# Performance work log

Hardware: AMD Instinct MI355X
Metric: run time of the kernel (lower is better)

The kernel has to match this reference:

```python
import jax, jax.numpy as jnp
import numpy as np

VAR_NUM, IN_DIM, OUT_DIM = 3, 8, 32
N_PTS, M_PTS, K_LAST = 8192, 2048, 10
RADIUS = 0.0342
PROJ_HIDDEN = 64
N_DIM = 2
MLP_DIMS = [2 * N_DIM + OUT_DIM, 80, 80, OUT_DIM]  # [36, 80, 80, 32]


def _gelu(x):
    # torch F.gelu default = exact erf form
    return jax.nn.gelu(x, approximate=False)


def _radius_neighbors(data, queries, r):
    # CSR-style neighbor lists (indices grouped per query), chunked for memory
    idx_chunks = []
    counts = np.zeros(queries.shape[0], np.int64)
    r2 = r * r
    for s in range(0, queries.shape[0], 1024):
        q = queries[s:s + 1024]
        d2 = ((q[:, None, :] - data[None, :, :]) ** 2).sum(-1)
        mask = d2 <= r2
        _, cols = np.nonzero(mask)  # row-major -> grouped by query
        idx_chunks.append(cols.astype(np.int32))
        counts[s:s + q.shape[0]] = mask.sum(1)
    return np.concatenate(idx_chunks), counts.astype(np.int32)


def _knn(data, queries, k):
    out = np.zeros((queries.shape[0], k), np.int32)
    for s in range(0, queries.shape[0], 1024):
        q = queries[s:s + 1024]
        d2 = ((q[:, None, :] - data[None, :, :]) ** 2).sum(-1)
        out[s:s + q.shape[0]] = np.argpartition(d2, k, axis=1)[:, :k]
    return out.reshape(-1)


def _mlp_params(key, dims):
    Ws, bs = [], []
    for i in range(len(dims) - 1):
        key, k1 = jax.random.split(key)
        Ws.append(jax.random.normal(k1, (dims[i], dims[i + 1]), jnp.float32) / np.sqrt(dims[i]).astype(np.float32))
        bs.append(jnp.zeros((dims[i + 1],), jnp.float32))
    return Ws, bs


def setup_inputs():
    rng = np.random.default_rng(0)
    input_grid = rng.uniform(size=(N_PTS, N_DIM)).astype(np.float32)
    output_grid = rng.uniform(size=(M_PTS, N_DIM)).astype(np.float32)
    nbr_index, nbr_counts = _radius_neighbors(input_grid, input_grid, RADIUS)
    nbr_seg = np.repeat(np.arange(N_PTS, dtype=np.int32), nbr_counts)
    nbr_last_index = _knn(input_grid, output_grid, K_LAST)

    key = jax.random.key(0)
    ks = jax.random.split(key, 4)
    inp = jax.random.normal(ks[0], (1, N_PTS, VAR_NUM * IN_DIM), jnp.float32)
    pW, pb = _mlp_params(ks[1], [IN_DIM, PROJ_HIDDEN, OUT_DIM])
    it0_W, it0_b = _mlp_params(ks[2], MLP_DIMS)
    it1_W, it1_b = _mlp_params(ks[3], MLP_DIMS)
    return dict(
        inp=inp,
        input_grid=jnp.asarray(input_grid), output_grid=jnp.asarray(output_grid),
        proj_W0=pW[0], proj_b0=pb[0], proj_W1=pW[1], proj_b1=pb[1],
        it0_W0=it0_W[0], it0_b0=it0_b[0], it0_W1=it0_W[1], it0_b1=it0_b[1], it0_W2=it0_W[2], it0_b2=it0_b[2],
        it1_W0=it1_W[0], it1_b0=it1_b[0], it1_W1=it1_W[1], it1_b1=it1_b[1], it1_W2=it1_W[2], it1_b2=it1_b[2],
        nbr_index=jnp.asarray(nbr_index), nbr_seg=jnp.asarray(nbr_seg),
        nbr_counts=jnp.asarray(nbr_counts), nbr_last_index=jnp.asarray(nbr_last_index),
    )


def _mlp3(x, W0, b0, W1, b1, W2, b2):
    x = _gelu(x @ W0 + b0)
    x = _gelu(x @ W1 + b1)
    return x @ W2 + b2


def reference(inp, input_grid, output_grid, proj_W0, proj_b0, proj_W1, proj_b1,
              it0_W0, it0_b0, it0_W1, it0_b1, it0_W2, it0_b2,
              it1_W0, it1_b0, it1_W1, it1_b1, it1_W2, it1_b2,
              nbr_index, nbr_seg, nbr_counts, nbr_last_index):
    B, N, _ = inp.shape  # B must be 1 (module's IT indexing assumes it)
    x = inp.reshape(B * N, VAR_NUM, IN_DIM)
    # pointwise projection MLP (gelu between layers)
    x = _gelu(x @ proj_W0 + proj_b0) @ proj_W1 + proj_b1  # (N, V, OUT_DIM)

    inv_counts = (1.0 / jnp.maximum(nbr_counts, 1).astype(x.dtype))[:, None]
    y_pos = input_grid[nbr_index]        # (E, 2) neighbor positions
    self_pos = input_grid[nbr_seg]       # (E, 2) query positions
    last_y = input_grid[nbr_last_index]                    # (M*K, 2)
    last_self = jnp.repeat(output_grid, K_LAST, axis=0)    # (M*K, 2)

    outs = []
    for v in range(VAR_NUM):
        f = x[:, v, :]
        # IT layer 0: radius neighborhoods on input grid, residual add
        agg = jnp.concatenate([y_pos, self_pos, f[nbr_index]], axis=-1)  # (E, 36)
        h = _mlp3(agg, it0_W0, it0_b0, it0_W1, it0_b1, it0_W2, it0_b2)
        f = jax.ops.segment_sum(h, nbr_seg, num_segments=N) * inv_counts + f
        # IT layer 1 (last): fixed-K neighbors from input grid to output grid, mean
        agg = jnp.concatenate([last_y, last_self, f[nbr_last_index]], axis=-1)
        h = _mlp3(agg, it1_W0, it1_b0, it1_W1, it1_b1, it1_W2, it1_b2)
        outs.append(h.reshape(M_PTS, K_LAST, OUT_DIM).mean(axis=1))
    # original concatenates temp[None] along dim=2 -> (1, M, V*OUT_DIM)
    return jnp.concatenate(outs, axis=-1)[None]
```

## Files before the change

kernel.cpp:

```cpp
#include <hip/hip_runtime.h>
#include <hip/hip_bf16.h>
#include <math.h>

#define N_PTS 8192
#define M_PTS 2048
#define KLAST 10
#define VARS 3
#define OUTD 32
#define D1 80
#define D2 80
#define PB 16
#define LPTS 4
#define NT 768
#define NWAVES 12
#define TPCH 104
#define W0P 72
#define W1P 104
#define RP 40

typedef float f4 __attribute__((ext_vector_type(4)));
typedef short bf16x8 __attribute__((ext_vector_type(8)));

__device__ __forceinline__ float gelu_f(float x) {
    float x2 = x * x;
    float t = x * (0.7978845608028654f + 0.0356774081f * x2);
    float u = __expf(2.0f * t);
    float th = 1.0f - 2.0f * __builtin_amdgcn_rcpf(u + 1.0f);
    return 0.5f * x * (1.0f + th);
}
__device__ __forceinline__ unsigned short f2bf(float x) {
    unsigned int u = __float_as_uint(x);
    u += 0x7FFF + ((u >> 16) & 1);
    return (unsigned short)(u >> 16);
}
__device__ __forceinline__ float bf2f(unsigned short h) {
    return __uint_as_float(((unsigned int)h) << 16);
}
__device__ __forceinline__ int pk2(float a, float b) {
    __hip_bfloat162 h = __float22bfloat162_rn(float2{a, b});
    int r; __builtin_memcpy(&r, &h, 4); return r;
}

__device__ __forceinline__ void stage_weights(
    unsigned short* W0h, unsigned short* W1h, unsigned short* W2h, float* bs,
    const float* __restrict__ W0g, const float* __restrict__ b0g,
    const float* __restrict__ W1g, const float* __restrict__ b1g,
    const float* __restrict__ W2g, const float* __restrict__ b2g, int t)
{
    for (int idx = t; idx < D1 * W0P; idx += NT) {
        int col = idx / W0P, k = idx - col * W0P;
        float w = (k < 32) ? W0g[(k + 4) * D1 + col]
                           : ((k < 36) ? W0g[(k - 32) * D1 + col] : 0.0f);
        W0h[idx] = f2bf(w);
    }
    for (int idx = t; idx < D1 * W1P; idx += NT) {
        int col = idx / W1P, k = idx - col * W1P;
        W1h[idx] = f2bf((k < D2) ? W1g[k * D1 + col] : 0.0f);
    }
    for (int idx = t; idx < OUTD * W1P; idx += NT) {
        int col = idx / W1P, k = idx - col * W1P;
        W2h[idx] = f2bf((k < D2) ? W2g[k * OUTD + col] : 0.0f);
    }
    for (int idx = t; idx < 192; idx += NT)
        bs[idx] = (idx < 80) ? b0g[idx] : (idx < 160 ? b1g[idx - 80] : b2g[idx - 160]);
}

__device__ __forceinline__ void mlp_chunk(
    int4 featsi, int4 posfi, unsigned short* Trow,
    const unsigned short* W0h, const unsigned short* W1h,
    const unsigned short* W2h, const float* bs, int lm, int quad)
{
    bf16x8 b1f0 = *(bf16x8*)&featsi;
    bf16x8 b1f1 = *(bf16x8*)&posfi;
#pragma unroll 1
    for (int cb = 0; cb < 5; ++cb) {
        f4 acc = *(const f4*)&bs[cb * 16 + quad * 4];
        bf16x8 a0 = *(const bf16x8*)&W0h[(cb * 16 + lm) * W0P + quad * 8];
        bf16x8 a1 = *(const bf16x8*)&W0h[(cb * 16 + lm) * W0P + 32 + quad * 8];
        acc = __builtin_amdgcn_mfma_f32_16x16x32_bf16(a0, b1f0, acc, 0, 0, 0);
        acc = __builtin_amdgcn_mfma_f32_16x16x32_bf16(a1, b1f1, acc, 0, 0, 0);
        *(int2*)&Trow[cb * 16 + quad * 4] =
            make_int2(pk2(gelu_f(acc.x), gelu_f(acc.y)),
                      pk2(gelu_f(acc.z), gelu_f(acc.w)));
    }
    bf16x8 b2f[3];
    b2f[0] = *(const bf16x8*)&Trow[quad * 8];
    b2f[1] = *(const bf16x8*)&Trow[32 + quad * 8];
    b2f[2] = *(const bf16x8*)&Trow[64 + quad * 8];
#pragma unroll 1
    for (int cb = 0; cb < 5; ++cb) {
        f4 acc = *(const f4*)&bs[80 + cb * 16 + quad * 4];
        const unsigned short* wh = &W1h[(cb * 16 + lm) * W1P + quad * 8];
        bf16x8 h0 = *(const bf16x8*)&wh[0];
        bf16x8 h1 = *(const bf16x8*)&wh[32];
        bf16x8 h2 = *(const bf16x8*)&wh[64];
        acc = __builtin_amdgcn_mfma_f32_16x16x32_bf16(h0, b2f[0], acc, 0, 0, 0);
        acc = __builtin_amdgcn_mfma_f32_16x16x32_bf16(h1, b2f[1], acc, 0, 0, 0);
        acc = __builtin_amdgcn_mfma_f32_16x16x32_bf16(h2, b2f[2], acc, 0, 0, 0);
        *(int2*)&Trow[cb * 16 + quad * 4] =
            make_int2(pk2(gelu_f(acc.x), gelu_f(acc.y)),
                      pk2(gelu_f(acc.z), gelu_f(acc.w)));
    }
    bf16x8 b3f[3];
    b3f[0] = *(const bf16x8*)&Trow[quad * 8];
    b3f[1] = *(const bf16x8*)&Trow[32 + quad * 8];
    b3f[2] = *(const bf16x8*)&Trow[64 + quad * 8];
    float* po = (float*)Trow;
#pragma unroll 1
    for (int cb = 0; cb < 2; ++cb) {
        f4 acc = *(const f4*)&bs[160 + cb * 16 + quad * 4];
        const unsigned short* wh = &W2h[(cb * 16 + lm) * W1P + quad * 8];
        bf16x8 h0 = *(const bf16x8*)&wh[0];
        bf16x8 h1 = *(const bf16x8*)&wh[32];
        bf16x8 h2 = *(const bf16x8*)&wh[64];
        acc = __builtin_amdgcn_mfma_f32_16x16x32_bf16(h0, b3f[0], acc, 0, 0, 0);
        acc = __builtin_amdgcn_mfma_f32_16x16x32_bf16(h1, b3f[1], acc, 0, 0, 0);
        acc = __builtin_amdgcn_mfma_f32_16x16x32_bf16(h2, b3f[2], acc, 0, 0, 0);
        *(f4*)&po[cb * 16 + quad * 4] = acc;
    }
}

__global__ __launch_bounds__(1024) void scan_kernel(
    const int* __restrict__ counts, int* __restrict__ offsets)
{
    __shared__ int wtot[16], wexc[16];
    const int t = threadIdx.x, lane = t & 63, wave = t >> 6;
    int4 a = ((const int4*)counts)[2 * t];
    int4 b = ((const int4*)counts)[2 * t + 1];
    int e1 = a.x, e2 = e1 + a.y, e3 = e2 + a.z, e4 = e3 + a.w;
    int e5 = e4 + b.x, e6 = e5 + b.y, e7 = e6 + b.z;
    int s = e7 + b.w;
    int x = s;
#pragma unroll
    for (int d = 1; d < 64; d <<= 1) {
        int y = __shfl_up(x, d);
        if (lane >= d) x += y;
    }
    if (lane == 63) wtot[wave] = x;
    int lane_base = x - s;
    __syncthreads();
    if (wave == 0 && lane < 16) {
        int v = wtot[lane];
        int xx = v;
#pragma unroll
        for (int d = 1; d < 16; d <<= 1) {
            int y = __shfl_up(xx, d);
            if (lane >= d) xx += y;
        }
        wexc[lane] = xx - v;
    }
    __syncthreads();
    int base = wexc[wave] + lane_base;
    ((int4*)offsets)[2 * t]     = make_int4(base, base + e1, base + e2, base + e3);
    ((int4*)offsets)[2 * t + 1] = make_int4(base + e4, base + e5, base + e6, base + e7);
}

__global__ __launch_bounds__(256) void proj_kernel(
    const float* __restrict__ inp, const float* __restrict__ grid_in,
    const float* __restrict__ W0, const float* __restrict__ b0,
    const float* __restrict__ W1, const float* __restrict__ b1,
    unsigned short* __restrict__ f0b)
{
    __shared__ float W0s[8 * 64];
    __shared__ float W1s[64 * OUTD];
    __shared__ float xs[32 * 8];
    __shared__ float H[32 * 64];
    const int t = threadIdx.x;
    const int r0 = blockIdx.x * 32;
    for (int idx = t; idx < 512; idx += 256) W0s[idx] = W0[idx];
    for (int idx = t; idx < 64 * OUTD; idx += 256) W1s[idx] = W1[idx];
    xs[t] = inp[r0 * 8 + t];
    if (t < 32) {
        int row = r0 + t, n = row / 3, v = row - n * 3;
        *(int*)(f0b + ((size_t)(v << 13) + n) * RP + 32) =
            pk2(grid_in[2 * n], grid_in[2 * n + 1]);
    }
    __syncthreads();
#pragma unroll 1
    for (int p = 0; p < 8; ++p) {
        int o = t + 256 * p, r = o >> 6, col = o & 63;
        float s = b0[col];
#pragma unroll
        for (int k = 0; k < 8; ++k) s += xs[r * 8 + k] * W0s[k * 64 + col];
        H[o] = gelu_f(s);
    }
    __syncthreads();
#pragma unroll 1
    for (int p = 0; p < 4; ++p) {
        int o = t + 256 * p, r = o >> 5, c = o & 31;
        float s = b1[c];
#pragma unroll 8
        for (int k = 0; k < 64; ++k) s += H[r * 64 + k] * W1s[k * OUTD + c];
        int row = r0 + r;
        int n = row / 3, v = row - n * 3;
        f0b[((size_t)(v << 13) + n) * RP + c] = f2bf(s);
    }
}

__global__ __launch_bounds__(768, 6) void agg_kernel(
    const float* __restrict__ grid_in, const unsigned short* __restrict__ f0b,
    const int* __restrict__ nbr_index, const int* __restrict__ offsets,
    const int* __restrict__ counts,
    const float* __restrict__ W0g, const float* __restrict__ b0g,
    const float* __restrict__ W1g, const float* __restrict__ b1g,
    const float* __restrict__ W2g, const float* __restrict__ b2g,
    unsigned short* __restrict__ f1b)
{
    __shared__ __attribute__((aligned(16))) unsigned short Tb[NWAVES * 16 * TPCH];
    __shared__ __attribute__((aligned(16))) unsigned short W0h[D1 * W0P];
    __shared__ __attribute__((aligned(16))) unsigned short W1h[D1 * W1P];
    __shared__ __attribute__((aligned(16))) unsigned short W2h[OUTD * W1P];
    __shared__ __attribute__((aligned(16))) float bs[192];
    __shared__ __attribute__((aligned(16))) float accH[VARS * PB * 32];
    __shared__ int offs[PB + 1];
    __shared__ int px2b[PB];
    __shared__ float invb[PB];

    const int t = threadIdx.x;
    const int lane = t & 63, wave = t >> 6;
    const int lm = lane & 15, quad = lane >> 4;
    const int p0 = blockIdx.x * PB;

    stage_weights(W0h, W1h, W2h, bs, W0g, b0g, W1g, b1g, W2g, b2g, t);
    if (t < PB) {
        offs[t] = offsets[p0 + t];
        int c = counts[p0 + t];
        invb[t] = 1.0f / (float)(c > 1 ? c : 1);
        px2b[t] = pk2(grid_in[2 * (p0 + t)], grid_in[2 * (p0 + t) + 1]);
    }
    if (t == PB) offs[PB] = offsets[p0 + PB - 1] + counts[p0 + PB - 1];
    for (int idx = t; idx < VARS * PB * 32; idx += NT) accH[idx] = 0.0f;
    __syncthreads();

    unsigned short* TbW = Tb + (wave * 16) * TPCH;
    if (lane < 32)
        *(int4*)(TbW + (lane >> 1) * TPCH + 80 + (lane & 1) * 8) = make_int4(0, 0, 0, 0);

    const int e0 = offs[0];
    const int cntT = offs[PB] - e0;
    const int Rb = VARS * cntT;
    const int nch = (Rb + 15) >> 4;

    unsigned short* Trow = TbW + lm * TPCH;

    int pkey; int4 pfeats, pposf;
    {
        int myrow = (wave << 4) + lm;
        pkey = -1; pfeats = make_int4(0,0,0,0); pposf = make_int4(0,0,0,0);
        if (myrow < Rb) {
            int myv = (myrow >= 2 * cntT) ? 2 : ((myrow >= cntT) ? 1 : 0);
            int e = e0 + myrow - myv * cntT;
            int myj = nbr_index[e];
            int lp = 0;
#pragma unroll
            for (int l = 1; l < PB; ++l) lp += (e >= offs[l]);
            pkey = myv * PB + lp;
            const unsigned short* rec = f0b + ((size_t)(myv << 13) + myj) * RP;
            pfeats = ((const int4*)rec)[quad];
            if (quad == 0) pposf = make_int4(*(const int*)(rec + 32), px2b[lp], 0, 0);
        }
    }

    for (int ch = wave; ch < nch; ch += NWAVES) {
        int ckey = pkey; int4 cfeats = pfeats, cposf = pposf;
        int nc = ch + NWAVES;
        pkey = -1; pfeats = make_int4(0,0,0,0); pposf = make_int4(0,0,0,0);
        if (nc < nch) {
            int myrow = (nc << 4) + lm;
            if (myrow < Rb) {
                int myv = (myrow >= 2 * cntT) ? 2 : ((myrow >= cntT) ? 1 : 0);
                int e = e0 + myrow - myv * cntT;
                int myj = nbr_index[e];
                int lp = 0;
#pragma unroll
                for (int l = 1; l < PB; ++l) lp += (e >= offs[l]);
                pkey = myv * PB + lp;
                const unsigned short* rec = f0b + ((size_t)(myv << 13) + myj) * RP;
                pfeats = ((const int4*)rec)[quad];
                if (quad == 0) pposf = make_int4(*(const int*)(rec + 32), px2b[lp], 0, 0);
            }
        }
        if (ckey < 0) { cfeats = make_int4(0,0,0,0); cposf = make_int4(0,0,0,0); }
        mlp_chunk(cfeats, cposf, Trow, W0h, W1h, W2h, bs, lm, quad);
        int col = lane & 31, eo = lane >> 5;
#pragma unroll 1
        for (int e2 = eo; e2 < 16; e2 += 2) {
            int k = __shfl(ckey, e2);
            if (k >= 0)
                atomicAdd(&accH[k * 32 + col], ((const float*)(TbW + e2 * TPCH))[col]);
        }
    }
    __syncthreads();
    for (int idx = t; idx < VARS * PB * OUTD; idx += NT) {
        int key = idx >> 5, c = idx & 31;
        int v = key >> 4, lp = key & 15;
        size_t rec = ((size_t)(v << 13) + p0 + lp) * RP;
        float val = accH[key * 32 + c] * invb[lp] + bf2f(f0b[rec + c]);
        f1b[rec + c] = f2bf(val);
    }
    if (t < VARS * PB) {
        int v = t >> 4, lp = t & 15;
        *(int*)(f1b + ((size_t)(v << 13) + p0 + lp) * RP + 32) = px2b[lp];
    }
}

__global__ __launch_bounds__(768, 6) void last_kernel(
    const unsigned short* __restrict__ f1b, const float* __restrict__ grid_out,
    const int* __restrict__ nbr_last,
    const float* __restrict__ W0g, const float* __restrict__ b0g,
    const float* __restrict__ W1g, const float* __restrict__ b1g,
    const float* __restrict__ W2g, const float* __restrict__ b2g,
    float* __restrict__ out)
{
    __shared__ __attribute__((aligned(16))) unsigned short Tb[NWAVES * 16 * TPCH];
    __shared__ __attribute__((aligned(16))) unsigned short W0h[D1 * W0P];
    __shared__ __attribute__((aligned(16))) unsigned short W1h[D1 * W1P];
    __shared__ __attribute__((aligned(16))) unsigned short W2h[OUTD * W1P];
    __shared__ __attribute__((aligned(16))) float bs[192];
    __shared__ __attribute__((aligned(16))) float accH[LPTS * VARS * 32];
    __shared__ int pxo2b[LPTS];

    const int t = threadIdx.x;
    const int lane = t & 63, wave = t >> 6;
    const int lm = lane & 15, quad = lane >> 4;
    const int m0 = blockIdx.x * LPTS;

    stage_weights(W0h, W1h, W2h, bs, W0g, b0g, W1g, b1g, W2g, b2g, t);
    if (t < LPTS)
        pxo2b[t] = pk2(grid_out[2 * (m0 + t)], grid_out[2 * (m0 + t) + 1]);
    for (int idx = t; idx < LPTS * VARS * 32; idx += NT) accH[idx] = 0.0f;
    __syncthreads();
    unsigned short* TbW = Tb + (wave * 16) * TPCH;
    if (lane < 32)
        *(int4*)(TbW + (lane >> 1) * TPCH + 80 + (lane & 1) * 8) = make_int4(0, 0, 0, 0);

    const int Rb = LPTS * VARS * KLAST;
    const int nch = (Rb + 15) >> 4;
    unsigned short* Trow = TbW + lm * TPCH;

    for (int ch = wave; ch < nch; ch += NWAVES) {
        int myrow = (ch << 4) + lm;
        int ckey = -1; int4 cfeats = make_int4(0,0,0,0), cposf = make_int4(0,0,0,0);
        if (myrow < Rb) {
            int lp = myrow / 30, rr = myrow - lp * 30;
            int v = rr / KLAST, kk = rr - v * KLAST;
            int myj = nbr_last[(m0 + lp) * KLAST + kk];
            ckey = lp * VARS + v;
            const unsigned short* rec = f1b + ((size_t)(v << 13) + myj) * RP;
            cfeats = ((const int4*)rec)[quad];
            if (quad == 0) cposf = make_int4(*(const int*)(rec + 32), pxo2b[lp], 0, 0);
        }
        mlp_chunk(cfeats, cposf, Trow, W0h, W1h, W2h, bs, lm, quad);
        int col = lane & 31, eo = lane >> 5;
#pragma unroll 1
        for (int e2 = eo; e2 < 16; e2 += 2) {
            int k = __shfl(ckey, e2);
            if (k >= 0)
                atomicAdd(&accH[k * 32 + col], ((const float*)(TbW + e2 * TPCH))[col]);
        }
    }
    __syncthreads();
    if (t < LPTS * VARS * OUTD) {
        int key = t >> 5, c = t & 31;
        int lp = key / VARS, v = key - lp * VARS;
        out[((size_t)(m0 + lp) * VARS + v) * OUTD + c] = accH[key * 32 + c] * (1.0f / KLAST);
    }
}

extern "C" void kernel_launch(void* const* d_in, const int* in_sizes, int n_in,
                              void* d_out, int out_size, void* d_ws, size_t ws_size,
                              hipStream_t stream) {
    const float* inp      = (const float*)d_in[0];
    const float* grid_in  = (const float*)d_in[1];
    const float* grid_out = (const float*)d_in[2];
    const float* pW0 = (const float*)d_in[3];
    const float* pb0 = (const float*)d_in[4];
    const float* pW1 = (const float*)d_in[5];
    const float* pb1 = (const float*)d_in[6];
    const float* i0W0 = (const float*)d_in[7];
    const float* i0b0 = (const float*)d_in[8];
    const float* i0W1 = (const float*)d_in[9];
    const float* i0b1 = (const float*)d_in[10];
    const float* i0W2 = (const float*)d_in[11];
    const float* i0b2 = (const float*)d_in[12];
    const float* i1W0 = (const float*)d_in[13];
    const float* i1b0 = (const float*)d_in[14];
    const float* i1W1 = (const float*)d_in[15];
    const float* i1b1 = (const float*)d_in[16];
    const float* i1W2 = (const float*)d_in[17];
    const float* i1b2 = (const float*)d_in[18];
    const int* nbr_index  = (const int*)d_in[19];
    const int* nbr_counts = (const int*)d_in[21];
    const int* nbr_last   = (const int*)d_in[22];

    unsigned short* f0b = (unsigned short*)d_ws;
    unsigned short* f1b = f0b + (size_t)VARS * N_PTS * RP;
    int* offsets = (int*)(f1b + (size_t)VARS * N_PTS * RP);

    proj_kernel<<<(N_PTS * VARS) / 32, 256, 0, stream>>>(inp, grid_in, pW0, pb0, pW1, pb1, f0b);
    scan_kernel<<<1, 1024, 0, stream>>>(nbr_counts, offsets);
    agg_kernel<<<N_PTS / PB, NT, 0, stream>>>(grid_in, f0b, nbr_index, offsets, nbr_counts,
                                              i0W0, i0b0, i0W1, i0b1, i0W2, i0b2, f1b);
    last_kernel<<<M_PTS / LPTS, NT, 0, stream>>>(f1b, grid_out, nbr_last,
                                                 i1W0, i1b0, i1W1, i1b1, i1W2, i1b2,
                                                 (float*)d_out);
}
```

Before: 338.1 us.

## Fuse scan into projection kernel, simplify GELU, double points per last block

Folds the prefix-scan of neighbor counts into an extra block of the projection kernel, removing one kernel launch. Rewrites the tanh-GELU approximation with exp2 and fewer operations. Increases LPTS from 4 to 8 so each last-layer block handles more output points, halving its grid. Risks: the last_kernel's indexing must still be valid for LPTS=8, and the scan block serializes 32 counts per thread.

```diff
diff --git a/kernel.cpp b/kernel.cpp
--- a/kernel.cpp
+++ b/kernel.cpp
@@ -10,7 +10,7 @@
 #define D1 80
 #define D2 80
 #define PB 16
-#define LPTS 4
+#define LPTS 8
 #define NT 768
 #define NWAVES 12
 #define TPCH 104
@@ -23,10 +23,10 @@
 
 __device__ __forceinline__ float gelu_f(float x) {
     float x2 = x * x;
-    float t = x * (0.7978845608028654f + 0.0356774081f * x2);
-    float u = __expf(2.0f * t);
-    float th = 1.0f - 2.0f * __builtin_amdgcn_rcpf(u + 1.0f);
-    return 0.5f * x * (1.0f + th);
+    float s = x * __builtin_fmaf(0.1029418f, x2, 2.3022083f);
+    float u = __builtin_amdgcn_exp2f(s);
+    float r = __builtin_amdgcn_rcpf(u + 1.0f);
+    return __builtin_fmaf(-x, r, x);
 }
 __device__ __forceinline__ unsigned short f2bf(float x) {
     unsigned int u = __float_as_uint(x);
@@ -120,52 +120,55 @@
     }
 }
 
-__global__ __launch_bounds__(1024) void scan_kernel(
-    const int* __restrict__ counts, int* __restrict__ offsets)
-{
-    __shared__ int wtot[16], wexc[16];
-    const int t = threadIdx.x, lane = t & 63, wave = t >> 6;
-    int4 a = ((const int4*)counts)[2 * t];
-    int4 b = ((const int4*)counts)[2 * t + 1];
-    int e1 = a.x, e2 = e1 + a.y, e3 = e2 + a.z, e4 = e3 + a.w;
-    int e5 = e4 + b.x, e6 = e5 + b.y, e7 = e6 + b.z;
-    int s = e7 + b.w;
-    int x = s;
-#pragma unroll
-    for (int d = 1; d < 64; d <<= 1) {
-        int y = __shfl_up(x, d);
-        if (lane >= d) x += y;
-    }
-    if (lane == 63) wtot[wave] = x;
-    int lane_base = x - s;
-    __syncthreads();
-    if (wave == 0 && lane < 16) {
-        int v = wtot[lane];
-        int xx = v;
-#pragma unroll
-        for (int d = 1; d < 16; d <<= 1) {
-            int y = __shfl_up(xx, d);
-            if (lane >= d) xx += y;
-        }
-        wexc[lane] = xx - v;
-    }
-    __syncthreads();
-    int base = wexc[wave] + lane_base;
-    ((int4*)offsets)[2 * t]     = make_int4(base, base + e1, base + e2, base + e3);
-    ((int4*)offsets)[2 * t + 1] = make_int4(base + e4, base + e5, base + e6, base + e7);
-}
-
-__global__ __launch_bounds__(256) void proj_kernel(
+__global__ __launch_bounds__(256) void proj_scan_kernel(
     const float* __restrict__ inp, const float* __restrict__ grid_in,
     const float* __restrict__ W0, const float* __restrict__ b0,
     const float* __restrict__ W1, const float* __restrict__ b1,
-    unsigned short* __restrict__ f0b)
+    unsigned short* __restrict__ f0b,
+    const int* __restrict__ counts, int* __restrict__ offsets)
 {
+    const int t = threadIdx.x;
+    if (blockIdx.x == 768) {
+        __shared__ int ws2[4], wx2[4];
+        const int lane = t & 63, wave = t >> 6;
+        int4 a[8];
+#pragma unroll
+        for (int i = 0; i < 8; ++i) a[i] = ((const int4*)counts)[t * 8 + i];
+        int s = 0;
+#pragma unroll
+        for (int i = 0; i < 8; ++i) s += a[i].x + a[i].y + a[i].z + a[i].w;
+        int x = s;
+#pragma unroll
+        for (int d = 1; d < 64; d <<= 1) {
+            int y = __shfl_up(x, d);
+            if (lane >= d) x += y;
+        }
+        if (lane == 63) ws2[wave] = x;
+        __syncthreads();
+        if (t == 0) {
+            wx2[0] = 0;
+            wx2[1] = ws2[0];
+            wx2[2] = ws2[0] + ws2[1];
+            wx2[3] = ws2[0] + ws2[1] + ws2[2];
+        }
+        __syncthreads();
+        int base = wx2[wave] + (x - s);
+#pragma unroll
+        for (int i = 0; i < 8; ++i) {
+            int4 c = a[i];
+            int4 o;
+            o.x = base; base += c.x;
+            o.y = base; base += c.y;
+            o.z = base; base += c.z;
+            o.w = base; base += c.w;
+            ((int4*)offsets)[t * 8 + i] = o;
+        }
+        return;
+    }
     __shared__ float W0s[8 * 64];
     __shared__ float W1s[64 * OUTD];
     __shared__ float xs[32 * 8];
     __shared__ float H[32 * 64];
-    const int t = threadIdx.x;
     const int r0 = blockIdx.x * 32;
     for (int idx = t; idx < 512; idx += 256) W0s[idx] = W0[idx];
     for (int idx = t; idx < 64 * OUTD; idx += 256) W1s[idx] = W1[idx];
@@ -397,9 +400,10 @@
     unsigned short* f1b = f0b + (size_t)VARS * N_PTS * RP;
     int* offsets = (int*)(f1b + (size_t)VARS * N_PTS * RP);
 
-    proj_kernel<<<(N_PTS * VARS) / 32, 256, 0, stream>>>(inp, grid_in, pW0, pb0, pW1, pb1, f0b);
-    scan_kernel<<<1, 1024, 0, stream>>>(nbr_counts, offsets);
-    agg_kernel<<<N_PTS / PB, NT, 0, stream>>>(grid_in, f0b, nbr_index, offsets, nbr_counts,
+    proj_scan_kernel<<<769, 256, 0, stream>>>(inp, grid_in, pW0, pb0, pW1, pb1,
+                                              f0b, nbr_counts, offsets);
+    agg_kernel<<<N_PTS / PB, NT, 0, stream>>>(grid_in, f0b, nbr_index, offsets,
+                                              nbr_counts,
                                               i0W0, i0b0, i0W1, i0b1, i0W2, i0b2, f1b);
     last_kernel<<<M_PTS / LPTS, NT, 0, stream>>>(f1b, grid_out, nbr_last,
                                                  i1W0, i1b0, i1W1, i1b1, i1W2, i1b2,
```

Result: faster. 329.3 us (-2.6%).
